# Optimization experiments

Measured on AMD Instinct MI355X. Metric: run time of the kernel, lower is better.

The kernel has to match this reference:

```python
import jax, jax.numpy as jnp
import numpy as np

B, D, L, NH = 8, 1024, 1024, 8
DK = D // NH  # = Dv = 128
NEG = -1e30


def setup_inputs() -> dict:
    key = jax.random.key(0)
    kx, km, kq, kk, kv, ko = jax.random.split(key, 6)
    x = jax.random.normal(kx, (B, D, L), dtype=jnp.float32)
    # binary mask over sequence positions (float, as in the torch code)
    mask = (jax.random.uniform(km, (B, L)) > 0.1).astype(jnp.float32)
    # xavier-ish scale for per-head projections, kaiming-ish for Wo
    s_qkv = np.sqrt(2.0 / (D + DK)).astype(np.float32)
    Wq = jax.random.normal(kq, (NH, D, DK), dtype=jnp.float32) * s_qkv
    Wk = jax.random.normal(kk, (NH, D, DK), dtype=jnp.float32) * s_qkv
    Wv = jax.random.normal(kv, (NH, D, DK), dtype=jnp.float32) * s_qkv
    Wo = jax.random.normal(ko, (D, DK * NH), dtype=jnp.float32) * np.sqrt(2.0 / D).astype(np.float32)
    return {"x": x, "mask": mask, "Wq": Wq, "Wk": Wk, "Wv": Wv, "Wo": Wo}


def reference(x, mask, Wq, Wk, Wv, Wo):
    # x: [B, D, L] -> [B, L, D]
    xt = jnp.swapaxes(x, 1, 2)
    scale = 1.0 / np.sqrt(DK).astype(np.float32)
    # batched per-head projections (equivalent to the per-head loop)
    q = jnp.einsum("bld,hdk->bhlk", xt, Wq)  # [B,H,L,Dk]
    k = jnp.einsum("bld,hdk->bhlk", xt, Wk)
    v = jnp.einsum("bld,hdk->bhlk", xt, Wv)
    # scores[b,h,q_pos,k_pos]
    scores = jnp.einsum("bhqd,bhkd->bhqk", q, k) * scale
    # mask.unsqueeze(2) in torch -> additive mask along the QUERY axis
    scores = scores + (1.0 - mask)[:, None, :, None] * NEG
    # faithful quirk: softmax over dim=1 of [B,Lq,Lk] == query axis (axis=2 here)
    attn = jax.nn.softmax(scores, axis=2)
    heads = jnp.einsum("bhqk,bhkd->bhqd", attn, v)  # [B,H,L,Dv]
    head = jnp.swapaxes(heads, 1, 2).reshape(B, L, NH * DK)  # concat heads
    out = head @ Wo  # [B, L, D]
    return jnp.swapaxes(out, 1, 2)  # [B, D, L]
```

## Files before the change

kernel.cpp:

```cpp
#include <hip/hip_runtime.h>

typedef short bf16x8 __attribute__((ext_vector_type(8)));
typedef float f32x4 __attribute__((ext_vector_type(4)));

#define MASK_NEG (-1e30f)

__device__ __forceinline__ unsigned short f2bf(float f) {
  union { float f; unsigned u; } v; v.f = f;
  unsigned r = v.u + 0x7fffu + ((v.u >> 16) & 1u);
  return (unsigned short)(r >> 16);
}

__device__ __forceinline__ void gl_lds16(const void* g, void* l) {
  __builtin_amdgcn_global_load_lds(
      (__attribute__((address_space(1))) void*)(void*)g,
      (__attribute__((address_space(3))) void*)l, 16, 0, 0);
}

__device__ __forceinline__ void transpose_tile(
    const float* __restrict__ s, unsigned short* __restrict__ d,
    int R, int C, int x0, int y0, int t, float tile[64][65]) {
  {
    const int r = t >> 4, c4 = (t & 15) * 4;
    for (int it = 0; it < 4; ++it) {
      const int rr = r + it * 16;
      const float4 v = *(const float4*)(s + (size_t)(y0 + rr) * C + x0 + c4);
      tile[rr][c4 + 0] = v.x; tile[rr][c4 + 1] = v.y;
      tile[rr][c4 + 2] = v.z; tile[rr][c4 + 3] = v.w;
    }
  }
  __syncthreads();
  {
    const int cc = t >> 4, r4 = (t & 15) * 4;
    for (int it = 0; it < 4; ++it) {
      const int c = cc + it * 16;
      ushort4 o;
      o.x = f2bf(tile[r4 + 0][c]); o.y = f2bf(tile[r4 + 1][c]);
      o.z = f2bf(tile[r4 + 2][c]); o.w = f2bf(tile[r4 + 3][c]);
      *(ushort4*)(d + (size_t)(x0 + c) * R + y0 + r4) = o;
    }
  }
}

__global__ __launch_bounds__(256) void transpose_x_wo(
    const float* __restrict__ x, const float* __restrict__ Wo,
    unsigned short* __restrict__ xt, unsigned short* __restrict__ Wot) {
  __shared__ float tile[64][65];
  const int z = blockIdx.z;
  const float* s = (z < 8) ? (x + (size_t)z * 1048576) : Wo;
  unsigned short* d = (z < 8) ? (xt + (size_t)z * 1048576) : Wot;
  transpose_tile(s, d, 1024, 1024, blockIdx.x * 64, blockIdx.y * 64,
                 threadIdx.x, tile);
}

__global__ __launch_bounds__(256) void transpose_w24(
    const float* __restrict__ Wq, const float* __restrict__ Wk,
    const float* __restrict__ Wv, unsigned short* __restrict__ WqkvT) {
  __shared__ float tile[64][65];
  const int z = blockIdx.z;
  const int sel = z >> 3, h = z & 7;
  const float* base = (sel == 0) ? Wq : (sel == 1) ? Wk : Wv;
  const float* s = base + (size_t)h * 131072;
  unsigned short* d = WqkvT + (size_t)z * 131072;
  transpose_tile(s, d, 1024, 128, blockIdx.x * 64, blockIdx.y * 64,
                 threadIdx.x, tile);
}

template<bool F32OUT>
__global__ __launch_bounds__(256) void gemm_tn(
    const unsigned short* __restrict__ A, const unsigned short* __restrict__ B,
    void* __restrict__ Cv,
    int K, int ldA, int ldB, int ldC, float scale,
    long sAl, long sAb, long sAh,
    long sBl, long sBb, long sBh,
    long sCl, long sCb, long sCh,
    int zbase, int zdiv, unsigned short* __restrict__ Vt)
{
  __shared__ unsigned short As[128 * 64];
  __shared__ unsigned short Bs[128 * 64];
  int bx, by, bz;
  {
    const int nx = gridDim.x, ny = gridDim.y;
    const int nwg = nx * ny * gridDim.z;
    int flat = blockIdx.x + nx * (blockIdx.y + ny * blockIdx.z);
    if ((nwg & 7) == 0) flat = (flat & 7) * (nwg >> 3) + (flat >> 3);
    bx = flat % nx; flat /= nx;
    by = flat % ny; bz = flat / ny;
  }
  const int z = bz;
  const int g = zbase + z;
  const int gb = g / zdiv, gh = g % zdiv;
  const unsigned short* Ab = A + (size_t)z * sAl + (size_t)gb * sAb + (size_t)gh * sAh;
  const unsigned short* Bb = B + (size_t)z * sBl + (size_t)gb * sBb + (size_t)gh * sBh;
  const int m0 = by * 128, n0 = bx * 128;
  const int t = threadIdx.x;
  const int lane = t & 63;
  const int wave = t >> 6;
  const int wm = wave >> 1, wn = wave & 1;

  const int sr2 = t >> 3;
  const int ss8 = t & 7;
  const int sq8 = ss8 ^ (sr2 & 7);

  const unsigned short* ap0 = Ab + (size_t)(m0 +  0 + sr2) * ldA + sq8 * 8;
  const unsigned short* ap1 = Ab + (size_t)(m0 + 32 + sr2) * ldA + sq8 * 8;
  const unsigned short* ap2 = Ab + (size_t)(m0 + 64 + sr2) * ldA + sq8 * 8;
  const unsigned short* ap3 = Ab + (size_t)(m0 + 96 + sr2) * ldA + sq8 * 8;
  const unsigned short* bp0 = Bb + (size_t)(n0 +  0 + sr2) * ldB + sq8 * 8;
  const unsigned short* bp1 = Bb + (size_t)(n0 + 32 + sr2) * ldB + sq8 * 8;
  const unsigned short* bp2 = Bb + (size_t)(n0 + 64 + sr2) * ldB + sq8 * 8;
  const unsigned short* bp3 = Bb + (size_t)(n0 + 96 + sr2) * ldB + sq8 * 8;

  char* asd0 = (char*)As +     0 + t * 16;
  char* asd1 = (char*)As +  4096 + t * 16;
  char* asd2 = (char*)As +  8192 + t * 16;
  char* asd3 = (char*)As + 12288 + t * 16;
  char* bsd0 = (char*)Bs +     0 + t * 16;
  char* bsd1 = (char*)Bs +  4096 + t * 16;
  char* bsd2 = (char*)Bs +  8192 + t * 16;
  char* bsd3 = (char*)Bs + 12288 + t * 16;

  const int tq = lane & 15, qd = lane >> 4;

  f32x4 acc[4][4];
  #pragma unroll
  for (int i = 0; i < 4; ++i)
    #pragma unroll
    for (int j = 0; j < 4; ++j)
      acc[i][j] = f32x4{0.f, 0.f, 0.f, 0.f};

  const int kIters = K >> 6;
  for (int kt = 0; kt < kIters; ++kt) {
    __syncthreads();
    gl_lds16(ap0, asd0); gl_lds16(ap1, asd1);
    gl_lds16(ap2, asd2); gl_lds16(ap3, asd3);
    gl_lds16(bp0, bsd0); gl_lds16(bp1, bsd1);
    gl_lds16(bp2, bsd2); gl_lds16(bp3, bsd3);
    ap0 += 64; ap1 += 64; ap2 += 64; ap3 += 64;
    bp0 += 64; bp1 += 64; bp2 += 64; bp3 += 64;
    __builtin_amdgcn_s_waitcnt(0x0f70);
    __syncthreads();

    #pragma unroll
    for (int kk = 0; kk < 2; ++kk) {
      bf16x8 af[4], bfr[4];
      #pragma unroll
      for (int i = 0; i < 4; ++i) {
        const int R = wm * 64 + i * 16 + tq;
        const int slot = (kk * 4 + qd) ^ (R & 7);
        af[i] = *(const bf16x8*)(As + R * 64 + slot * 8);
      }
      #pragma unroll
      for (int j = 0; j < 4; ++j) {
        const int R = wn * 64 + j * 16 + tq;
        const int slot = (kk * 4 + qd) ^ (R & 7);
        bfr[j] = *(const bf16x8*)(Bs + R * 64 + slot * 8);
      }
      #pragma unroll
      for (int i = 0; i < 4; ++i)
        #pragma unroll
        for (int j = 0; j < 4; ++j)
          acc[i][j] = __builtin_amdgcn_mfma_f32_16x16x32_bf16(af[i], bfr[j], acc[i][j], 0, 0, 0);
    }
  }

  if (!F32OUT && Vt != nullptr && gh >= 16) {
    unsigned short* Vb = Vt + (size_t)(gb * 8 + (gh - 16)) * 131072;
    #pragma unroll
    for (int i = 0; i < 4; ++i) {
      const int row = m0 + wm * 64 + i * 16 + qd * 4;
      #pragma unroll
      for (int j = 0; j < 4; ++j) {
        const int col = n0 + wn * 64 + j * 16 + tq;
        ushort4 o;
        o.x = f2bf(acc[i][j][0] * scale);
        o.y = f2bf(acc[i][j][1] * scale);
        o.z = f2bf(acc[i][j][2] * scale);
        o.w = f2bf(acc[i][j][3] * scale);
        *(ushort4*)(Vb + (size_t)col * 1024 + row) = o;
      }
    }
    return;
  }

  const size_t cOff = (size_t)z * sCl + (size_t)gb * sCb + (size_t)gh * sCh;
  #pragma unroll
  for (int i = 0; i < 4; ++i) {
    const int row = m0 + wm * 64 + i * 16 + qd * 4;
    #pragma unroll
    for (int j = 0; j < 4; ++j) {
      const int col = n0 + wn * 64 + j * 16 + tq;
      if constexpr (F32OUT) {
        float* C = (float*)Cv + cOff;
        #pragma unroll
        for (int rr = 0; rr < 4; ++rr)
          C[(size_t)(row + rr) * ldC + col] = acc[i][j][rr] * scale;
      } else {
        unsigned short* C = (unsigned short*)Cv + cOff;
        #pragma unroll
        for (int rr = 0; rr < 4; ++rr)
          C[(size_t)(row + rr) * ldC + col] = f2bf(acc[i][j][rr] * scale);
      }
    }
  }
}

__global__ __launch_bounds__(256, 2) void scores_colsum(
    const unsigned short* __restrict__ QKV, float* __restrict__ colsum,
    const float* __restrict__ mask)
{
  __shared__ unsigned short lds[24576];
  __shared__ float csacc[2][1024];
  unsigned short* Qs = lds;

  const int bid = blockIdx.x;
  const int w = ((bid & 7) << 6) | (bid >> 3);
  const int g = w >> 3, qx = w & 7;
  const int b = g >> 3, h = g & 7;
  const unsigned short* Qg = QKV + (size_t)b * 3145728 + (size_t)h * 131072
                                 + (size_t)qx * 16384;
  const unsigned short* Kg = QKV + (size_t)b * 3145728 + (size_t)(8 + h) * 131072;

  const int t = threadIdx.x;
  const int lane = t & 63, wave = t >> 6;
  const int wm = wave >> 1, wn = wave & 1;
  const int tq = lane & 15, qd = lane >> 4;

  #pragma unroll
  for (int it = 0; it < 8; ++it) {
    const int c = it * 256 + t;
    const int row = c >> 4;
    const int src = (c ^ (c >> 4)) & 15;
    gl_lds16(Qg + (size_t)row * 128 + src * 8, (char*)Qs + c * 16);
  }
  #pragma unroll
  for (int it = 0; it < 4; ++it) {
    const int c = it * 256 + t;
    const int row = c >> 4;
    const int src = (c ^ (c >> 4)) & 15;
    gl_lds16(Kg + (size_t)row * 128 + src * 8, (char*)(lds + 16384) + c * 16);
  }
  __builtin_amdgcn_s_waitcnt(0x0f70);
  __syncthreads();

  bf16x8 qf[4][4];
  #pragma unroll
  for (int i = 0; i < 4; ++i) {
    const int R = wm * 64 + i * 16 + tq;
    #pragma unroll
    for (int kk = 0; kk < 4; ++kk)
      qf[i][kk] = *(const bf16x8*)(Qs + R * 128 + (((kk * 4 + qd) ^ (R & 15)) * 8));
  }
  __syncthreads();

  const float scl = 0.08838834764831845f;
  float aq[4][4];
  {
    const float* mrow = mask + (size_t)b * 1024 + qx * 128;
    #pragma unroll
    for (int i = 0; i < 4; ++i) {
      const float4 m4 = *(const float4*)(mrow + wm * 64 + i * 16 + qd * 4);
      aq[i][0] = (1.f - m4.x) * MASK_NEG - 20.f;
      aq[i][1] = (1.f - m4.y) * MASK_NEG - 20.f;
      aq[i][2] = (1.f - m4.z) * MASK_NEG - 20.f;
      aq[i][3] = (1.f - m4.w) * MASK_NEG - 20.f;
    }
  }

  for (int kt = 0; kt < 16; ++kt) {
    __builtin_amdgcn_s_barrier();
    if (kt < 15) {
      unsigned short* Kn = ((kt + 1) & 1) ? lds : (lds + 16384);
      const unsigned short* Kgn = Kg + (size_t)(kt + 1) * 8192;
      #pragma unroll
      for (int it = 0; it < 4; ++it) {
        const int c = it * 256 + t;
        const int row = c >> 4;
        const int src = (c ^ (c >> 4)) & 15;
        gl_lds16(Kgn + (size_t)row * 128 + src * 8, (char*)Kn + c * 16);
      }
      asm volatile("s_waitcnt vmcnt(4)" ::: "memory");
    } else {
      asm volatile("s_waitcnt vmcnt(0)" ::: "memory");
    }
    __builtin_amdgcn_s_barrier();

    const unsigned short* Kc = (kt & 1) ? lds : (lds + 16384);
    f32x4 acc_s[4][2];
    #pragma unroll
    for (int i = 0; i < 4; ++i)
      #pragma unroll
      for (int j = 0; j < 2; ++j)
        acc_s[i][j] = f32x4{0.f, 0.f, 0.f, 0.f};
    #pragma unroll
    for (int kk = 0; kk < 4; ++kk) {
      bf16x8 kf[2];
      #pragma unroll
      for (int j = 0; j < 2; ++j) {
        const int R = wn * 32 + j * 16 + tq;
        kf[j] = *(const bf16x8*)(Kc + R * 128 + (((kk * 4 + qd) ^ (R & 15)) * 8));
      }
      #pragma unroll
      for (int i = 0; i < 4; ++i)
        #pragma unroll
        for (int j = 0; j < 2; ++j)
          acc_s[i][j] = __builtin_amdgcn_mfma_f32_16x16x32_bf16(qf[i][kk], kf[j], acc_s[i][j], 0, 0, 0);
    }

    float cp0 = 0.f, cp1 = 0.f;
    #pragma unroll
    for (int i = 0; i < 4; ++i)
      #pragma unroll
      for (int rr = 0; rr < 4; ++rr) {
        cp0 += __expf(acc_s[i][0][rr] * scl + aq[i][rr]);
        cp1 += __expf(acc_s[i][1][rr] * scl + aq[i][rr]);
      }
    cp0 += __shfl_xor(cp0, 16, 64); cp0 += __shfl_xor(cp0, 32, 64);
    cp1 += __shfl_xor(cp1, 16, 64); cp1 += __shfl_xor(cp1, 32, 64);
    if (qd == 0) {
      csacc[wm][kt * 64 + wn * 32 + tq] = cp0;
      csacc[wm][kt * 64 + wn * 32 + 16 + tq] = cp1;
    }
  }

  __syncthreads();
  float* cs = colsum + (size_t)g * 1024;
  #pragma unroll
  for (int r = 0; r < 4; ++r) {
    const int idx = r * 256 + t;
    atomicAdd(&cs[idx], csacc[0][idx] + csacc[1][idx]);
  }
}

__global__ __launch_bounds__(256, 2) void attn_pv_fused(
    const unsigned short* __restrict__ QKV, const unsigned short* __restrict__ Vp,
    unsigned short* __restrict__ Hp, const float* __restrict__ mask,
    const float* __restrict__ colsum)
{
  __shared__ unsigned short lds[40960];
  unsigned short* Ps = lds;
  unsigned short* Qs = lds;

  const int bid = blockIdx.x;
  const int w = ((bid & 7) << 6) | (bid >> 3);
  const int g = w >> 3, qx = w & 7;
  const int b = g >> 3, h = g & 7;
  const unsigned short* Qg = QKV + (size_t)b * 3145728 + (size_t)h * 131072
                                 + (size_t)qx * 16384;
  const unsigned short* Kg = QKV + (size_t)b * 3145728 + (size_t)(8 + h) * 131072;
  const unsigned short* Vg = Vp + (size_t)g * 131072;

  const int t = threadIdx.x;
  const int lane = t & 63, wave = t >> 6;
  const int wm = wave >> 1, wn = wave & 1;
  const int tq = lane & 15, qd = lane >> 4;

  #pragma unroll
  for (int it = 0; it < 8; ++it) {
    const int c = it * 256 + t;
    const int row = c >> 4;
    const int src = (c ^ (c >> 4)) & 15;
    gl_lds16(Qg + (size_t)row * 128 + src * 8, (char*)Qs + c * 16);
  }
  #pragma unroll
  for (int it = 0; it < 4; ++it) {
    const int c = it * 256 + t;
    const int row = c >> 4;
    const int src = (c ^ (c >> 4)) & 15;
    gl_lds16(Kg + (size_t)row * 128 + src * 8, (char*)(lds + 16384) + c * 16);
  }
  #pragma unroll
  for (int it = 0; it < 4; ++it) {
    const int c = it * 256 + t;
    const int row = c >> 3;
    const int src = (c ^ (c >> 3)) & 7;
    gl_lds16(Vg + (size_t)row * 1024 + src * 8, (char*)(lds + 24576) + c * 16);
  }
  __builtin_amdgcn_s_waitcnt(0x0f70);
  __syncthreads();

  bf16x8 qf[4][4];
  #pragma unroll
  for (int i = 0; i < 4; ++i) {
    const int R = wm * 64 + i * 16 + tq;
    #pragma unroll
    for (int kk = 0; kk < 4; ++kk)
      qf[i][kk] = *(const bf16x8*)(Qs + R * 128 + (((kk * 4 + qd) ^ (R & 15)) * 8));
  }
  __syncthreads();

  f32x4 acc_h[4][4];
  #pragma unroll
  for (int i = 0; i < 4; ++i)
    #pragma unroll
    for (int j = 0; j < 4; ++j)
      acc_h[i][j] = f32x4{0.f, 0.f, 0.f, 0.f};

  const float scl = 0.08838834764831845f;
  float aq[4][4];
  {
    const float* mrow = mask + (size_t)b * 1024 + qx * 128;
    #pragma unroll
    for (int i = 0; i < 4; ++i) {
      const float4 m4 = *(const float4*)(mrow + wm * 64 + i * 16 + qd * 4);
      aq[i][0] = (1.f - m4.x) * MASK_NEG - 20.f;
      aq[i][1] = (1.f - m4.y) * MASK_NEG - 20.f;
      aq[i][2] = (1.f - m4.z) * MASK_NEG - 20.f;
      aq[i][3] = (1.f - m4.w) * MASK_NEG - 20.f;
    }
  }
  const float* cs = colsum + (size_t)g * 1024;

  for (int kt = 0; kt < 16; ++kt) {
    __builtin_amdgcn_s_barrier();
    if (kt < 15) {
      unsigned short* Kn = ((kt + 1) & 1) ? (lds + 8192) : (lds + 16384);
      unsigned short* Vn = ((kt + 1) & 1) ? (lds + 32768) : (lds + 24576);
      const unsigned short* Kgn = Kg + (size_t)(kt + 1) * 8192;
      #pragma unroll
      for (int it = 0; it < 4; ++it) {
        const int c = it * 256 + t;
        const int row = c >> 4;
        const int src = (c ^ (c >> 4)) & 15;
        gl_lds16(Kgn + (size_t)row * 128 + src * 8, (char*)Kn + c * 16);
      }
      #pragma unroll
      for (int it = 0; it < 4; ++it) {
        const int c = it * 256 + t;
        const int row = c >> 3;
        const int src = (c ^ (c >> 3)) & 7;
        gl_lds16(Vg + (size_t)row * 1024 + (kt + 1) * 64 + src * 8, (char*)Vn + c * 16);
      }
      asm volatile("s_waitcnt vmcnt(12)" ::: "memory");
    } else {
      asm volatile("s_waitcnt vmcnt(4)" ::: "memory");
    }
    __builtin_amdgcn_s_barrier();

    const unsigned short* Kc = (kt & 1) ? (lds + 8192) : (lds + 16384);
    const unsigned short* Vc = (kt & 1) ? (lds + 32768) : (lds + 24576);

    f32x4 acc_s[4][2];
    #pragma unroll
    for (int i = 0; i < 4; ++i)
      #pragma unroll
      for (int j = 0; j < 2; ++j)
        acc_s[i][j] = f32x4{0.f, 0.f, 0.f, 0.f};
    #pragma unroll
    for (int kk = 0; kk < 4; ++kk) {
      bf16x8 kf[2];
      #pragma unroll
      for (int j = 0; j < 2; ++j) {
        const int R = wn * 32 + j * 16 + tq;
        kf[j] = *(const bf16x8*)(Kc + R * 128 + (((kk * 4 + qd) ^ (R & 15)) * 8));
      }
      #pragma unroll
      for (int i = 0; i < 4; ++i)
        #pragma unroll
        for (int j = 0; j < 2; ++j)
          acc_s[i][j] = __builtin_amdgcn_mfma_f32_16x16x32_bf16(qf[i][kk], kf[j], acc_s[i][j], 0, 0, 0);
    }

    const float rcs0 = 1.0f / cs[kt * 64 + wn * 32 + tq];
    const float rcs1 = 1.0f / cs[kt * 64 + wn * 32 + 16 + tq];
    #pragma unroll
    for (int i = 0; i < 4; ++i) {
      const int q0 = wm * 64 + i * 16 + qd * 4;
      #pragma unroll
      for (int rr = 0; rr < 4; ++rr) {
        const int q = q0 + rr;
        #pragma unroll
        for (int j = 0; j < 2; ++j) {
          const int kl = wn * 32 + j * 16 + tq;
          const float e = __expf(acc_s[i][j][rr] * scl + aq[i][rr]) * (j ? rcs1 : rcs0);
          Ps[q * 64 + ((((kl >> 3) ^ (q & 7)) * 8) | (kl & 7))] = f2bf(e);
        }
      }
    }
    if (kt < 15)
      asm volatile("s_waitcnt vmcnt(8) lgkmcnt(0)" ::: "memory");
    else
      asm volatile("s_waitcnt vmcnt(0) lgkmcnt(0)" ::: "memory");
    __builtin_amdgcn_s_barrier();

    #pragma unroll
    for (int k2 = 0; k2 < 2; ++k2) {
      bf16x8 pf[4], vf[4];
      #pragma unroll
      for (int i = 0; i < 4; ++i) {
        const int R = wm * 64 + i * 16 + tq;
        pf[i] = *(const bf16x8*)(Ps + R * 64 + (((k2 * 4 + qd) ^ (R & 7)) * 8));
      }
      #pragma unroll
      for (int j = 0; j < 4; ++j) {
        const int R = wn * 64 + j * 16 + tq;
        vf[j] = *(const bf16x8*)(Vc + R * 64 + (((k2 * 4 + qd) ^ (R & 7)) * 8));
      }
      #pragma unroll
      for (int i = 0; i < 4; ++i)
        #pragma unroll
        for (int j = 0; j < 4; ++j)
          acc_h[i][j] = __builtin_amdgcn_mfma_f32_16x16x32_bf16(pf[i], vf[j], acc_h[i][j], 0, 0, 0);
    }
  }

  unsigned short* Hb = Hp + (size_t)b * 1048576 + (size_t)qx * 131072 + h * 128;
  #pragma unroll
  for (int i = 0; i < 4; ++i) {
    const int q0 = wm * 64 + i * 16 + qd * 4;
    #pragma unroll
    for (int j = 0; j < 4; ++j) {
      const int dv = wn * 64 + j * 16 + tq;
      #pragma unroll
      for (int rr = 0; rr < 4; ++rr)
        Hb[(size_t)(q0 + rr) * 1024 + dv] = f2bf(acc_h[i][j][rr]);
    }
  }
}

extern "C" void kernel_launch(void* const* d_in, const int* in_sizes, int n_in,
                              void* d_out, int out_size, void* d_ws, size_t ws_size,
                              hipStream_t stream) {
  const float* x    = (const float*)d_in[0];
  const float* mask = (const float*)d_in[1];
  const float* Wq   = (const float*)d_in[2];
  const float* Wk   = (const float*)d_in[3];
  const float* Wv   = (const float*)d_in[4];
  const float* Wo   = (const float*)d_in[5];
  float* out = (float*)d_out;

  char* p = (char*)d_ws;
  unsigned short* xt    = (unsigned short*)p; p += 16777216;
  unsigned short* WqkvT = (unsigned short*)p; p += 6291456;
  unsigned short* Wot   = (unsigned short*)p; p += 2097152;
  unsigned short* QKV   = (unsigned short*)p; p += 50331648;
  unsigned short* Vp    = (unsigned short*)p; p += 16777216;
  unsigned short* Hp    = (unsigned short*)p; p += 16777216;
  float* colsum = (float*)p; p += 262144;

  hipMemsetAsync(colsum, 0, 262144, stream);

  transpose_x_wo<<<dim3(16, 16, 9), 256, 0, stream>>>(x, Wo, xt, Wot);
  transpose_w24<<<dim3(2, 16, 24), 256, 0, stream>>>(Wq, Wk, Wv, WqkvT);

  gemm_tn<false><<<dim3(1, 8, 192), 256, 0, stream>>>(
      xt, WqkvT, (void*)QKV, 1024, 1024, 1024, 128, 1.f,
      0L, 1048576L, 0L,  0L, 0L, 131072L,  0L, 3145728L, 131072L, 0, 24, Vp);

  scores_colsum<<<dim3(512, 1, 1), 256, 0, stream>>>(QKV, colsum, mask);

  attn_pv_fused<<<dim3(512, 1, 1), 256, 0, stream>>>(QKV, Vp, Hp, mask, colsum);

  gemm_tn<true><<<dim3(8, 8, 8), 256, 0, stream>>>(
      Wot, Hp, (void*)out, 1024, 1024, 1024, 1024, 1.f,
      0L, 0L, 0L,  0L, 1048576L, 0L,  0L, 1048576L, 0L, 0, 1, nullptr);
}
```

Measured before the change: 277.5 us.

## Fold column-sum normalization into V and add scheduling priorities

Moves the per-key softmax normalization (division by the column sum) out of the attention inner loop. A new vnorm kernel pre-scales the transposed V by 1/colsum and writes it into the unused V slot of QKV, so attn_pv_fused no longer loads colsum or multiplies P by reciprocals. The change also adds sched_barrier fences around the block barriers and raises wave priority around the MFMA sections. The cost is an extra kernel launch with a full read and write of V, plus an extra bf16 rounding of the normalized V.

```diff
diff --git a/kernel.cpp b/kernel.cpp
--- a/kernel.cpp
+++ b/kernel.cpp
@@ -2,6 +2,7 @@
 
 typedef short bf16x8 __attribute__((ext_vector_type(8)));
 typedef float f32x4 __attribute__((ext_vector_type(4)));
+typedef unsigned short u16x8 __attribute__((ext_vector_type(8)));
 
 #define MASK_NEG (-1e30f)
 
@@ -9,6 +10,11 @@
   union { float f; unsigned u; } v; v.f = f;
   unsigned r = v.u + 0x7fffu + ((v.u >> 16) & 1u);
   return (unsigned short)(r >> 16);
+}
+
+__device__ __forceinline__ float bf2f(unsigned short u) {
+  union { unsigned u; float f; } v; v.u = ((unsigned)u) << 16;
+  return v.f;
 }
 
 __device__ __forceinline__ void gl_lds16(const void* g, void* l) {
@@ -269,6 +275,7 @@
 
   for (int kt = 0; kt < 16; ++kt) {
     __builtin_amdgcn_s_barrier();
+    __builtin_amdgcn_sched_barrier(0);
     if (kt < 15) {
       unsigned short* Kn = ((kt + 1) & 1) ? lds : (lds + 16384);
       const unsigned short* Kgn = Kg + (size_t)(kt + 1) * 8192;
@@ -284,6 +291,7 @@
       asm volatile("s_waitcnt vmcnt(0)" ::: "memory");
     }
     __builtin_amdgcn_s_barrier();
+    __builtin_amdgcn_sched_barrier(0);
 
     const unsigned short* Kc = (kt & 1) ? lds : (lds + 16384);
     f32x4 acc_s[4][2];
@@ -292,6 +300,7 @@
       #pragma unroll
       for (int j = 0; j < 2; ++j)
         acc_s[i][j] = f32x4{0.f, 0.f, 0.f, 0.f};
+    __builtin_amdgcn_s_setprio(1);
     #pragma unroll
     for (int kk = 0; kk < 4; ++kk) {
       bf16x8 kf[2];
@@ -306,6 +315,7 @@
         for (int j = 0; j < 2; ++j)
           acc_s[i][j] = __builtin_amdgcn_mfma_f32_16x16x32_bf16(qf[i][kk], kf[j], acc_s[i][j], 0, 0, 0);
     }
+    __builtin_amdgcn_s_setprio(0);
 
     float cp0 = 0.f, cp1 = 0.f;
     #pragma unroll
@@ -332,10 +342,31 @@
   }
 }
 
+__global__ __launch_bounds__(256) void vnorm(
+    const unsigned short* __restrict__ Vpu, unsigned short* __restrict__ QKV,
+    const float* __restrict__ colsum)
+{
+  const int g = blockIdx.y;
+  const int b = g >> 3, h = g & 7;
+  const unsigned short* S = Vpu + (size_t)g * 131072;
+  unsigned short* D = QKV + (size_t)b * 3145728 + (size_t)(16 + h) * 131072;
+  const float* cs = colsum + (size_t)g * 1024;
+  const int off = (blockIdx.x * 256 + threadIdx.x) * 8;
+  const int l0 = off & 1023;
+  const u16x8 v = *(const u16x8*)(S + off);
+  const float4 c0 = *(const float4*)(cs + l0);
+  const float4 c1 = *(const float4*)(cs + l0 + 4);
+  u16x8 o;
+  o[0] = f2bf(bf2f(v[0]) / c0.x); o[1] = f2bf(bf2f(v[1]) / c0.y);
+  o[2] = f2bf(bf2f(v[2]) / c0.z); o[3] = f2bf(bf2f(v[3]) / c0.w);
+  o[4] = f2bf(bf2f(v[4]) / c1.x); o[5] = f2bf(bf2f(v[5]) / c1.y);
+  o[6] = f2bf(bf2f(v[6]) / c1.z); o[7] = f2bf(bf2f(v[7]) / c1.w);
+  *(u16x8*)(D + off) = o;
+}
+
 __global__ __launch_bounds__(256, 2) void attn_pv_fused(
-    const unsigned short* __restrict__ QKV, const unsigned short* __restrict__ Vp,
-    unsigned short* __restrict__ Hp, const float* __restrict__ mask,
-    const float* __restrict__ colsum)
+    const unsigned short* __restrict__ QKV,
+    unsigned short* __restrict__ Hp, const float* __restrict__ mask)
 {
   __shared__ unsigned short lds[40960];
   unsigned short* Ps = lds;
@@ -348,7 +379,7 @@
   const unsigned short* Qg = QKV + (size_t)b * 3145728 + (size_t)h * 131072
                                  + (size_t)qx * 16384;
   const unsigned short* Kg = QKV + (size_t)b * 3145728 + (size_t)(8 + h) * 131072;
-  const unsigned short* Vg = Vp + (size_t)g * 131072;
+  const unsigned short* Vg = QKV + (size_t)b * 3145728 + (size_t)(16 + h) * 131072;
 
   const int t = threadIdx.x;
   const int lane = t & 63, wave = t >> 6;
@@ -409,10 +440,10 @@
       aq[i][3] = (1.f - m4.w) * MASK_NEG - 20.f;
     }
   }
-  const float* cs = colsum + (size_t)g * 1024;
 
   for (int kt = 0; kt < 16; ++kt) {
     __builtin_amdgcn_s_barrier();
+    __builtin_amdgcn_sched_barrier(0);
     if (kt < 15) {
       unsigned short* Kn = ((kt + 1) & 1) ? (lds + 8192) : (lds + 16384);
       unsigned short* Vn = ((kt + 1) & 1) ? (lds + 32768) : (lds + 24576);
@@ -436,6 +467,7 @@
       asm volatile("s_waitcnt vmcnt(4)" ::: "memory");
     }
     __builtin_amdgcn_s_barrier();
+    __builtin_amdgcn_sched_barrier(0);
 
     const unsigned short* Kc = (kt & 1) ? (lds + 8192) : (lds + 16384);
     const unsigned short* Vc = (kt & 1) ? (lds + 32768) : (lds + 24576);
@@ -446,6 +478,7 @@
       #pragma unroll
       for (int j = 0; j < 2; ++j)
         acc_s[i][j] = f32x4{0.f, 0.f, 0.f, 0.f};
+    __builtin_amdgcn_s_setprio(1);
     #pragma unroll
     for (int kk = 0; kk < 4; ++kk) {
       bf16x8 kf[2];
@@ -460,9 +493,8 @@
         for (int j = 0; j < 2; ++j)
           acc_s[i][j] = __builtin_amdgcn_mfma_f32_16x16x32_bf16(qf[i][kk], kf[j], acc_s[i][j], 0, 0, 0);
     }
-
-    const float rcs0 = 1.0f / cs[kt * 64 + wn * 32 + tq];
-    const float rcs1 = 1.0f / cs[kt * 64 + wn * 32 + 16 + tq];
+    __builtin_amdgcn_s_setprio(0);
+
     #pragma unroll
     for (int i = 0; i < 4; ++i) {
       const int q0 = wm * 64 + i * 16 + qd * 4;
@@ -472,7 +504,7 @@
         #pragma unroll
         for (int j = 0; j < 2; ++j) {
           const int kl = wn * 32 + j * 16 + tq;
-          const float e = __expf(acc_s[i][j][rr] * scl + aq[i][rr]) * (j ? rcs1 : rcs0);
+          const float e = __expf(acc_s[i][j][rr] * scl + aq[i][rr]);
           Ps[q * 64 + ((((kl >> 3) ^ (q & 7)) * 8) | (kl & 7))] = f2bf(e);
         }
       }
@@ -482,7 +514,9 @@
     else
       asm volatile("s_waitcnt vmcnt(0) lgkmcnt(0)" ::: "memory");
     __builtin_amdgcn_s_barrier();
-
+    __builtin_amdgcn_sched_barrier(0);
+
+    __builtin_amdgcn_s_setprio(1);
     #pragma unroll
     for (int k2 = 0; k2 < 2; ++k2) {
       bf16x8 pf[4], vf[4];
@@ -502,6 +536,7 @@
         for (int j = 0; j < 4; ++j)
           acc_h[i][j] = __builtin_amdgcn_mfma_f32_16x16x32_bf16(pf[i], vf[j], acc_h[i][j], 0, 0, 0);
     }
+    __builtin_amdgcn_s_setprio(0);
   }
 
   unsigned short* Hb = Hp + (size_t)b * 1048576 + (size_t)qx * 131072 + h * 128;
@@ -534,7 +569,7 @@
   unsigned short* WqkvT = (unsigned short*)p; p += 6291456;
   unsigned short* Wot   = (unsigned short*)p; p += 2097152;
   unsigned short* QKV   = (unsigned short*)p; p += 50331648;
-  unsigned short* Vp    = (unsigned short*)p; p += 16777216;
+  unsigned short* Vpu   = (unsigned short*)p; p += 16777216;
   unsigned short* Hp    = (unsigned short*)p; p += 16777216;
   float* colsum = (float*)p; p += 262144;
 
@@ -545,11 +580,13 @@
 
   gemm_tn<false><<<dim3(1, 8, 192), 256, 0, stream>>>(
       xt, WqkvT, (void*)QKV, 1024, 1024, 1024, 128, 1.f,
-      0L, 1048576L, 0L,  0L, 0L, 131072L,  0L, 3145728L, 131072L, 0, 24, Vp);
+      0L, 1048576L, 0L,  0L, 0L, 131072L,  0L, 3145728L, 131072L, 0, 24, Vpu);
 
   scores_colsum<<<dim3(512, 1, 1), 256, 0, stream>>>(QKV, colsum, mask);
 
-  attn_pv_fused<<<dim3(512, 1, 1), 256, 0, stream>>>(QKV, Vp, Hp, mask, colsum);
+  vnorm<<<dim3(64, 64, 1), 256, 0, stream>>>(Vpu, QKV, colsum);
+
+  attn_pv_fused<<<dim3(512, 1, 1), 256, 0, stream>>>(QKV, Hp, mask);
 
   gemm_tn<true><<<dim3(8, 8, 8), 256, 0, stream>>>(
       Wot, Hp, (void*)out, 1024, 1024, 1024, 1024, 1.f,
```

New measurement: 267.8 us. -3.5%, faster.
